# Kernel tuning notes

Measured on AMD Instinct MI355X. Metric: run time of the kernel, lower is better.

The kernel has to match this reference:

```python
import jax, jax.numpy as jnp
import numpy as np

B, R, NB, T = 32, 96, 5, 2048
FEAT_DIM = 64
SPARSITY = 0.2


def _per_band(X, community, W1, b1, W2, b2):
    # X: [R, T] wavelet coeffs for one (batch, band) slice
    n, t = X.shape
    f32 = X.dtype
    # --- functional connectivity (cosine of centered signals == Pearson corr) ---
    Xc = X - X.mean(axis=1, keepdims=True)
    norm = jnp.linalg.norm(Xc, axis=1, keepdims=True)
    norm = jnp.where(norm == 0, 1.0, norm)
    C = (Xc @ Xc.T) / (norm * norm.T)
    C = jnp.nan_to_num(C, nan=0.0)
    C = C * (1.0 - jnp.eye(n, dtype=f32))  # zero diagonal
    # --- quantile sparsification over strict lower triangle ---
    ti, tj = np.tril_indices(n, -1)
    thr = jnp.quantile(jnp.abs(C[ti, tj]), 1.0 - SPARSITY)
    A = C * (jnp.abs(C) >= thr).astype(f32)  # graph_type == 'weighted'
    # --- node features (5-dim, averaged over regions) ---
    mean_f = X.mean(axis=1)
    std_f = jnp.std(X, axis=1, ddof=1)  # torch.std is unbiased
    energy_f = (X ** 2).sum(axis=1)
    maxamp_f = jnp.abs(X).max(axis=1)
    ps = jnp.abs(jnp.fft.fft(X, axis=1)) ** 2
    ps = ps[:, : t // 2]
    s = ps.sum(axis=1, keepdims=True)
    s = jnp.where(s == 0, 1.0, s)
    p = ps / s
    ent_f = -(p * jnp.log(p + 1e-10)).sum(axis=1)
    node5 = jnp.stack([mean_f, std_f, energy_f, maxamp_f, ent_f], axis=1).mean(axis=0)
    # --- graph properties (6-dim) on binarized adjacency ---
    Bm = (A != 0).astype(f32)
    ne = Bm.sum() / 2.0
    density = ne / (n * (n - 1) / 2.0)
    deg = Bm.sum(axis=1)
    avg_deg = deg.mean()
    A2 = Bm @ Bm
    tri = (A2 * Bm).sum() / 6.0
    poss = (deg * (deg - 1.0)).sum() / 2.0
    clus = jnp.where(poss > 0, tri / jnp.where(poss > 0, poss, 1.0), 0.0)
    # global efficiency: safe reciprocal (zero where A+I == 0; original would emit inf)
    denom = Bm + jnp.eye(n, dtype=f32)
    eff = jnp.where(denom > 0, 1.0 / jnp.where(denom > 0, denom, 1.0), 0.0).sum() / (n * (n - 1))
    # approximate modularity with fixed 2-community assignment (deterministic)
    m2 = 2.0 * ne
    m2_safe = jnp.where(m2 > 0, m2, 1.0)
    same = (community[:, None] == community[None, :]) & (~jnp.eye(n, dtype=bool))
    expected = jnp.outer(deg, deg) / m2_safe
    mod = jnp.where(m2 > 0, (same * (Bm - expected)).sum() / m2_safe, 0.0)
    props = jnp.stack([ne, density, avg_deg, clus, eff, mod])
    feat11 = jnp.concatenate([node5, props])  # [11]
    # --- feature encoder MLP (dropout is identity at inference) ---
    h = jnp.maximum(feat11 @ W1.T + b1, 0.0)
    return A, h @ W2.T + b2


def _forward(wavelet_coeffs, frequency_bands, community, W1, b1, W2, b2):
    b, r, nb, t = wavelet_coeffs.shape
    Xs = wavelet_coeffs.transpose(0, 2, 1, 3).reshape(b * nb, r, t)  # [B*NB, R, T]
    A, F = jax.vmap(_per_band, in_axes=(0, None, None, None, None, None))(
        Xs, community, W1, b1, W2, b2)
    return A.reshape(b, nb, r, r), F.reshape(b, nb, -1)


def setup_inputs() -> dict:
    key = jax.random.key(0)
    k0, k1, k2, k3, k4 = jax.random.split(key, 5)
    wavelet_coeffs = jax.random.normal(k0, (B, R, NB, T), dtype=jnp.float32)
    frequency_bands = jax.random.uniform(k1, (NB, 2), dtype=jnp.float32)
    community = jax.random.randint(k2, (R,), 0, 2)
    W1 = jax.random.normal(k3, (32, 11), dtype=jnp.float32) * 0.3
    b1 = jnp.zeros((32,), jnp.float32)
    W2 = jax.random.normal(k4, (FEAT_DIM, 32), dtype=jnp.float32) * 0.18
    b2 = jnp.zeros((FEAT_DIM,), jnp.float32)
    return {"wavelet_coeffs": wavelet_coeffs, "frequency_bands": frequency_bands,
            "community": community, "W1": W1, "b1": b1, "W2": W2, "b2": b2}


def reference(wavelet_coeffs, frequency_bands, community, W1, b1, W2, b2):
    return _forward(wavelet_coeffs, frequency_bands, community, W1, b1, W2, b2)
```

## Files before the change

### kernel.cpp

```cpp
#include <hip/hip_runtime.h>
#include <hip/hip_bf16.h>
#include <math.h>
#include <float.h>

#ifndef M_PI
#define M_PI 3.14159265358979323846
#endif

#define NBANDS 160
#define RR 96
#define TT 2048
#define NTRIL 4560
#define A_ELEMS ((size_t)NBANDS * RR * RR)
#define NBIN 8192
#define MAXCAND 512
#define BKS 64
#define GPITCH 72
#define FBLK 384

#define PHI(L) ((L) ^ (((L) >> 5) & 31))

typedef float  f32x4  __attribute__((ext_vector_type(4)));
typedef __bf16 bf16x8 __attribute__((ext_vector_type(8)));
typedef __bf16 bf16x4 __attribute__((ext_vector_type(4)));

__device__ inline void blockReduceSum4(double v0, double v1, double v2, double v3,
                                       double* sred, double out[4]) {
    for (int off = 32; off > 0; off >>= 1) {
        v0 += __shfl_down(v0, off, 64);
        v1 += __shfl_down(v1, off, 64);
        v2 += __shfl_down(v2, off, 64);
        v3 += __shfl_down(v3, off, 64);
    }
    int lane = threadIdx.x & 63, wid = threadIdx.x >> 6;
    int nw = blockDim.x >> 6;
    if (lane == 0) {
        sred[wid * 4 + 0] = v0; sred[wid * 4 + 1] = v1;
        sred[wid * 4 + 2] = v2; sred[wid * 4 + 3] = v3;
    }
    __syncthreads();
    if (threadIdx.x < 4) {
        double r = sred[threadIdx.x];
        for (int w = 1; w < nw; w++) r += sred[w * 4 + threadIdx.x];
        sred[nw * 4 + threadIdx.x] = r;
    }
    __syncthreads();
    out[0] = sred[nw * 4 + 0]; out[1] = sred[nw * 4 + 1];
    out[2] = sred[nw * 4 + 2]; out[3] = sred[nw * 4 + 3];
    __syncthreads();
}

__device__ inline void blockReduceSum2(double v0, double v1,
                                       double* sred, double out[2]) {
    for (int off = 32; off > 0; off >>= 1) {
        v0 += __shfl_down(v0, off, 64);
        v1 += __shfl_down(v1, off, 64);
    }
    int lane = threadIdx.x & 63, wid = threadIdx.x >> 6;
    int nw = blockDim.x >> 6;
    if (lane == 0) { sred[wid * 2 + 0] = v0; sred[wid * 2 + 1] = v1; }
    __syncthreads();
    if (threadIdx.x < 2) {
        double r = sred[threadIdx.x];
        for (int w = 1; w < nw; w++) r += sred[w * 2 + threadIdx.x];
        sred[nw * 2 + threadIdx.x] = r;
    }
    __syncthreads();
    out[0] = sred[nw * 2 + 0]; out[1] = sred[nw * 2 + 1];
    __syncthreads();
}

__device__ inline void blockReduceMax2(double v0, double v1,
                                       double* sred, double out[2]) {
    for (int off = 32; off > 0; off >>= 1) {
        v0 = fmax(v0, __shfl_down(v0, off, 64));
        v1 = fmax(v1, __shfl_down(v1, off, 64));
    }
    int lane = threadIdx.x & 63, wid = threadIdx.x >> 6;
    int nw = blockDim.x >> 6;
    if (lane == 0) { sred[wid * 2 + 0] = v0; sred[wid * 2 + 1] = v1; }
    __syncthreads();
    if (threadIdx.x < 2) {
        double r = sred[threadIdx.x];
        for (int w = 1; w < nw; w++) r = fmax(r, sred[w * 2 + threadIdx.x]);
        sred[nw * 2 + threadIdx.x] = r;
    }
    __syncthreads();
    out[0] = sred[nw * 2 + 0]; out[1] = sred[nw * 2 + 1];
    __syncthreads();
}

__global__ void twiddle_kernel(float* tw) {
    int k = blockIdx.x * blockDim.x + threadIdx.x;
    if (k < 1024) {
        double ang = -2.0 * M_PI * (double)k / 2048.0;
        tw[2 * k]     = (float)cos(ang);
        tw[2 * k + 1] = (float)sin(ang);
    }
}

#define BFLY(r1, r2, WR, WI) do { \
    float _wr = (WR), _wi = (WI); \
    float _tr = _wr * yr[r2] - _wi * yi[r2]; \
    float _ti = _wr * yi[r2] + _wi * yr[r2]; \
    yr[r2] = yr[r1] - _tr; yi[r2] = yi[r1] - _ti; \
    yr[r1] += _tr; yi[r1] += _ti; } while (0)

__global__ __launch_bounds__(256) void rowstat_fft_kernel(
    const float* __restrict__ wc, const float* __restrict__ tw,
    double* __restrict__ rowstats)
{
    __shared__ float re[TT];
    __shared__ float im[TT];
    __shared__ double sred[32];
    __shared__ float bcast[4];

    int t = threadIdx.x;
    int g0 = blockIdx.x * 2;
    int g1 = g0 + 1;

    int band = g0 / RR, r0 = g0 % RR;
    int b = band / 5, nb = band % 5;
    size_t base0 = ((size_t)(b * RR + r0) * 5 + nb) * TT;
    size_t base1 = base0 + (size_t)5 * TT;
    const float2* twv = (const float2*)tw;

    float s0 = 0.f, s1 = 0.f, q0 = 0.f, q1 = 0.f, m0 = 0.f, m1 = 0.f;
#pragma unroll
    for (int c = 0; c < 8; c++) {
        int i = t + c * 256;
        float af = wc[base0 + i];
        float bf = wc[base1 + i];
        int P = PHI(i);
        re[P] = af; im[P] = bf;
        s0 += af; s1 += bf;
        q0 = fmaf(af, af, q0); q1 = fmaf(bf, bf, q1);
        m0 = fmaxf(m0, fabsf(af)); m1 = fmaxf(m1, fabsf(bf));
    }
    __syncthreads();

    double S4[4], M2[2];
    blockReduceSum4((double)s0, (double)s1, (double)q0, (double)q1, sred, S4);
    blockReduceMax2((double)m0, (double)m1, sred, M2);
    double SUM0 = S4[0], SUM1 = S4[1], SQ0 = S4[2], SQ1 = S4[3];
    double MX0 = M2[0], MX1 = M2[1];

    float yr[8], yi[8];

#pragma unroll
    for (int j = 0; j < 8; j++) {
        int p = 8 * t + j;
        int L = (int)(__brev((unsigned)p) >> 21);
        int P = PHI(L);
        yr[j] = re[P]; yi[j] = im[P];
    }

    const float RC = 0.70710678f;
    BFLY(0, 1, 1.0f, 0.0f); BFLY(2, 3, 1.0f, 0.0f);
    BFLY(4, 5, 1.0f, 0.0f); BFLY(6, 7, 1.0f, 0.0f);
    BFLY(0, 2, 1.0f, 0.0f); BFLY(1, 3, 0.0f, -1.0f);
    BFLY(4, 6, 1.0f, 0.0f); BFLY(5, 7, 0.0f, -1.0f);
    BFLY(0, 4, 1.0f, 0.0f); BFLY(1, 5, RC, -RC);
    BFLY(2, 6, 0.0f, -1.0f); BFLY(3, 7, -RC, -RC);

    __syncthreads();
#pragma unroll
    for (int j = 0; j < 8; j++) {
        int P = PHI(8 * t + j);
        re[P] = yr[j]; im[P] = yi[j];
    }
    __syncthreads();
    int oo = t & 7;
    int bb64 = 4 * ((t >> 3) & 7) + (t >> 6);
#pragma unroll
    for (int k = 0; k < 8; k++) {
        int P = PHI(64 * bb64 + 8 * k + oo);
        yr[k] = re[P]; yi[k] = im[P];
    }

    {
        float2 w0 = twv[oo << 7];
        BFLY(0, 1, w0.x, w0.y); BFLY(2, 3, w0.x, w0.y);
        BFLY(4, 5, w0.x, w0.y); BFLY(6, 7, w0.x, w0.y);
        float2 wa = twv[oo << 6];
        float2 wb = twv[(oo + 8) << 6];
        BFLY(0, 2, wa.x, wa.y); BFLY(1, 3, wb.x, wb.y);
        BFLY(4, 6, wa.x, wa.y); BFLY(5, 7, wb.x, wb.y);
        float2 wc0 = twv[oo << 5], wc1 = twv[(oo + 8) << 5];
        float2 wc2 = twv[(oo + 16) << 5], wc3 = twv[(oo + 24) << 5];
        BFLY(0, 4, wc0.x, wc0.y);
        BFLY(1, 5, wc1.x, wc1.y);
        BFLY(2, 6, wc2.x, wc2.y);
        BFLY(3, 7, wc3.x, wc3.y);
    }

    __syncthreads();
#pragma unroll
    for (int k = 0; k < 8; k++) {
        int P = PHI(64 * bb64 + 8 * k + oo);
        re[P] = yr[k]; im[P] = yi[k];
    }
    __syncthreads();
    int O3 = t & 63, Wq = t >> 6;
#pragma unroll
    for (int s = 0; s < 2; s++) {
        int B3 = Wq + 4 * s;
#pragma unroll
        for (int k = 0; k < 4; k++) {
            int P = PHI(256 * B3 + 64 * k + O3);
            yr[4 * s + k] = re[P]; yi[4 * s + k] = im[P];
        }
    }

    {
        float2 w0 = twv[O3 << 4];
        float2 wa = twv[O3 << 3];
        float2 wb = twv[(O3 + 64) << 3];
        BFLY(0, 1, w0.x, w0.y); BFLY(2, 3, w0.x, w0.y);
        BFLY(4, 5, w0.x, w0.y); BFLY(6, 7, w0.x, w0.y);
        BFLY(0, 2, wa.x, wa.y); BFLY(1, 3, wb.x, wb.y);
        BFLY(4, 6, wa.x, wa.y); BFLY(5, 7, wb.x, wb.y);
    }

    __syncthreads();
#pragma unroll
    for (int s = 0; s < 2; s++) {
        int B3 = Wq + 4 * s;
#pragma unroll
        for (int k = 0; k < 4; k++) {
            int P = PHI(256 * B3 + 64 * k + O3);
            re[P] = yr[4 * s + k]; im[P] = yi[4 * s + k];
        }
    }
    __syncthreads();
#pragma unroll
    for (int k = 0; k < 8; k++) {
        int P = PHI(256 * k + t);
        yr[k] = re[P]; yi[k] = im[P];
    }

    {
        float2 w0 = twv[t << 2];
        float2 wa = twv[t << 1];
        float2 wb = twv[(t + 256) << 1];
        BFLY(0, 1, w0.x, w0.y); BFLY(2, 3, w0.x, w0.y);
        BFLY(4, 5, w0.x, w0.y); BFLY(6, 7, w0.x, w0.y);
        BFLY(0, 2, wa.x, wa.y); BFLY(1, 3, wb.x, wb.y);
        BFLY(4, 6, wa.x, wa.y); BFLY(5, 7, wb.x, wb.y);
        float2 wf0 = twv[t], wf1 = twv[t + 256];
        float2 wf2 = twv[t + 512], wf3 = twv[t + 768];
        BFLY(0, 4, wf0.x, wf0.y);
        BFLY(1, 5, wf1.x, wf1.y);
        BFLY(2, 6, wf2.x, wf2.y);
        BFLY(3, 7, wf3.x, wf3.y);
    }

    __syncthreads();
#pragma unroll
    for (int k = 0; k < 8; k++) {
        int P = PHI(256 * k + t);
        re[P] = yr[k]; im[P] = yi[k];
    }
    __syncthreads();

    float psa[8], psb[8];
#pragma unroll
    for (int k = 0; k < 8; k++) {
        int q = (2048 - t - 256 * k) & 2047;
        int P = PHI(q);
        float prr = re[P], pii = im[P];
        float sr = yr[k] + prr, di = yi[k] - pii;
        float si = yi[k] + pii, dr = yr[k] - prr;
        psa[k] = 0.25f * (sr * sr + di * di);
        psb[k] = 0.25f * (si * si + dr * dr);
    }

    float la = 0.f, lb = 0.f;
#pragma unroll
    for (int k = 0; k < 8; k++) { la += psa[k]; lb += psb[k]; }
    double SS[2];
    blockReduceSum2((double)la, (double)lb, sred, SS);
    double SAall = SS[0], SBall = SS[1];
    if (t == 0) {
        bcast[0] = psa[0]; bcast[1] = psa[4];
        bcast[2] = psb[0]; bcast[3] = psb[4];
    }
    __syncthreads();
    double Sa = 0.5 * (SAall + (double)bcast[0] - (double)bcast[1]);
    double Sb = 0.5 * (SBall + (double)bcast[2] - (double)bcast[3]);
    if (Sa == 0.0) Sa = 1.0;
    if (Sb == 0.0) Sb = 1.0;
    float invSa = (float)(1.0 / Sa), invSb = (float)(1.0 / Sb);

    float ea = 0.f, eb = 0.f;
#pragma unroll
    for (int k = 0; k < 8; k++) {
        float pa = psa[k] * invSa;
        float pb = psb[k] * invSb;
        ea += pa * __logf(pa + 1e-10f);
        eb += pb * __logf(pb + 1e-10f);
    }
    double EE[2];
    blockReduceSum2((double)ea, (double)eb, sred, EE);
    double EAall = EE[0], EBall = EE[1];

    if (t == 0) {
        float pa0 = psa[0] * invSa, pa4 = psa[4] * invSa;
        float pb0 = psb[0] * invSb, pb4 = psb[4] * invSb;
        double TA = 0.5 * (EAall + (double)(pa0 * __logf(pa0 + 1e-10f))
                                 - (double)(pa4 * __logf(pa4 + 1e-10f)));
        double TB = 0.5 * (EBall + (double)(pb0 * __logf(pb0 + 1e-10f))
                                 - (double)(pb4 * __logf(pb4 + 1e-10f)));
        double mean0 = SUM0 / (double)TT;
        double mean1 = SUM1 / (double)TT;
        double nsq0 = SQ0 - (double)TT * mean0 * mean0; if (nsq0 < 0) nsq0 = 0;
        double nsq1 = SQ1 - (double)TT * mean1 * mean1; if (nsq1 < 0) nsq1 = 0;
        double* w0 = rowstats + (size_t)g0 * 6;
        double* w1 = rowstats + (size_t)g1 * 6;
        double n0 = sqrt(nsq0), n1 = sqrt(nsq1);
        w0[0] = mean0; w0[1] = (n0 == 0.0 ? 1.0 : n0); w0[2] = sqrt(nsq0 / 2047.0);
        w0[3] = SQ0;   w0[4] = MX0;                    w0[5] = -TA;
        w1[0] = mean1; w1[1] = (n1 == 0.0 ? 1.0 : n1); w1[2] = sqrt(nsq1 / 2047.0);
        w1[3] = SQ1;   w1[4] = MX1;                    w1[5] = -TB;
    }
}

#define CVW(v, row, c4) do { \
    __bf16 _h0 = (__bf16)v.x, _h1 = (__bf16)v.y, _h2 = (__bf16)v.z, _h3 = (__bf16)v.w; \
    __bf16 _l0 = (__bf16)(v.x - (float)_h0), _l1 = (__bf16)(v.y - (float)_h1); \
    __bf16 _l2 = (__bf16)(v.z - (float)_h2), _l3 = (__bf16)(v.w - (float)_h3); \
    *(bf16x4*)&sh_hi[row][(c4) * 4] = (bf16x4){_h0, _h1, _h2, _h3}; \
    *(bf16x4*)&sh_lo[row][(c4) * 4] = (bf16x4){_l0, _l1, _l2, _l3}; } while (0)

__global__ __launch_bounds__(FBLK) void fused_gram_finalize_kernel(
    const float* __restrict__ wc, const double* __restrict__ rowstats,
    const int* __restrict__ community,
    const float* __restrict__ W1, const float* __restrict__ b1,
    const float* __restrict__ W2, const float* __restrict__ b2,
    float* __restrict__ A_out, float* __restrict__ F_out)
{
    __shared__ __attribute__((aligned(16))) __bf16 sh_hi[RR][GPITCH];
    __shared__ __attribute__((aligned(16))) __bf16 sh_lo[RR][GPITCH];
    __shared__ float Cs[RR][RR];
    __shared__ int hist[NBIN];
    __shared__ int chunkv[256];
    __shared__ float cand[MAXCAND];
    __shared__ int ctrl[4];
    __shared__ double mean_s[RR], inv_s[RR];
    __shared__ int comm_s[RR];
    __shared__ unsigned long long msk[RR][2];
    __shared__ int deg[RR];
    __shared__ double sred[32];
    __shared__ double feat[11];
    __shared__ double hmlp[32];
    __shared__ double thr_s;

    int band = blockIdx.x, t = threadIdx.x;
    int b = band / 5, nb = band % 5;
    size_t bandbase = ((size_t)b * RR * 5 + nb) * TT;
    const double* rsb = rowstats + (size_t)band * RR * 6;

    if (t < RR) {
        mean_s[t] = rsb[t * 6 + 0];
        inv_s[t]  = 1.0 / rsb[t * 6 + 1];
        comm_s[t] = community[t];
    }
    for (int i = t; i < NBIN; i += FBLK) hist[i] = 0;
    if (t == 0) ctrl[3] = 0;

    int wave = t >> 6, lane = t & 63;
    int m16 = lane & 15, quad = lane >> 4;
    int arow = wave * 16 + m16;

    int gid0 = t, gid1 = t + 384, gid2 = t + 768, gid3 = t + 1152;
    int row0 = gid0 >> 4, c40 = gid0 & 15;
    int row1 = gid1 >> 4, c41 = gid1 & 15;
    int row2 = gid2 >> 4, c42 = gid2 & 15;
    int row3 = gid3 >> 4, c43 = gid3 & 15;
    const float* p0 = wc + bandbase + (size_t)row0 * (5 * TT) + c40 * 4;
    const float* p1 = wc + bandbase + (size_t)row1 * (5 * TT) + c41 * 4;
    const float* p2 = wc + bandbase + (size_t)row2 * (5 * TT) + c42 * 4;
    const float* p3 = wc + bandbase + (size_t)row3 * (5 * TT) + c43 * 4;

    f32x4 acc[6];
#pragma unroll
    for (int ct = 0; ct < 6; ct++) acc[ct] = (f32x4){0.f, 0.f, 0.f, 0.f};

    float4 pr0 = *(const float4*)(p0);
    float4 pr1 = *(const float4*)(p1);
    float4 pr2 = *(const float4*)(p2);
    float4 pr3 = *(const float4*)(p3);

    for (int st = 0; st < TT / BKS; st++) {
        CVW(pr0, row0, c40); CVW(pr1, row1, c41);
        CVW(pr2, row2, c42); CVW(pr3, row3, c43);
        __syncthreads();
        if (st + 1 < TT / BKS) {
            int k0 = (st + 1) * BKS;
            pr0 = *(const float4*)(p0 + k0);
            pr1 = *(const float4*)(p1 + k0);
            pr2 = *(const float4*)(p2 + k0);
            pr3 = *(const float4*)(p3 + k0);
        }
#pragma unroll
        for (int ks = 0; ks < BKS / 32; ks++) {
            int ko = ks * 32 + quad * 8;
            bf16x8 ah = *(const bf16x8*)&sh_hi[arow][ko];
            bf16x8 al = *(const bf16x8*)&sh_lo[arow][ko];
#pragma unroll
            for (int ct = 0; ct < 6; ct++) {
                int brow = ct * 16 + m16;
                bf16x8 bh = *(const bf16x8*)&sh_hi[brow][ko];
                bf16x8 bl = *(const bf16x8*)&sh_lo[brow][ko];
                acc[ct] = __builtin_amdgcn_mfma_f32_16x16x32_bf16(ah, bh, acc[ct], 0, 0, 0);
                acc[ct] = __builtin_amdgcn_mfma_f32_16x16x32_bf16(ah, bl, acc[ct], 0, 0, 0);
                acc[ct] = __builtin_amdgcn_mfma_f32_16x16x32_bf16(al, bh, acc[ct], 0, 0, 0);
            }
        }
        __syncthreads();
    }

#pragma unroll
    for (int ct = 0; ct < 6; ct++) {
#pragma unroll
        for (int r = 0; r < 4; r++) {
            int grow = wave * 16 + quad * 4 + r;
            int gcol = ct * 16 + m16;
            double cd = ((double)acc[ct][r]
                         - (double)TT * mean_s[grow] * mean_s[gcol])
                        * (inv_s[grow] * inv_s[gcol]);
            if (grow == gcol) cd = 0.0;
            float cf = (float)cd;
            Cs[grow][gcol] = cf;
            if (gcol < grow) {
                float val = fabsf(cf);
                int bin = (int)(val * (float)NBIN);
                bin = bin > (NBIN - 1) ? (NBIN - 1) : bin;
                atomicAdd(&hist[bin], 1);
            }
        }
    }
    __syncthreads();

    if (t < 256) {
        int cs = 0;
        for (int i = 0; i < NBIN / 256; i++) cs += hist[t * (NBIN / 256) + i];
        chunkv[t] = cs;
    }
    __syncthreads();

    if (t == 0) {
        int r0 = 3647, r1 = 3648;
        int cum = 0, c0 = 0;
        while (c0 < 256 && cum + chunkv[c0] <= r0) { cum += chunkv[c0]; c0++; }
        int bin = c0 * (NBIN / 256), cb = cum;
        while (cb + hist[bin] <= r0) { cb += hist[bin]; bin++; }
        int B0 = bin, cumB0 = cb;
        int bin1 = bin, cb1 = cb;
        while (cb1 + hist[bin1] <= r1) { cb1 += hist[bin1]; bin1++; }
        ctrl[0] = B0; ctrl[1] = bin1; ctrl[2] = cumB0;
    }
    __syncthreads();

    int B0 = ctrl[0], B1 = ctrl[1];
    for (int idx = t; idx < RR * RR; idx += FBLK) {
        int i = idx / RR, j = idx % RR;
        if (j < i) {
            float val = fabsf(Cs[i][j]);
            int bin = (int)(val * (float)NBIN);
            bin = bin > (NBIN - 1) ? (NBIN - 1) : bin;
            if (bin >= B0 && bin <= B1) {
                int k = atomicAdd(&ctrl[3], 1);
                if (k < MAXCAND) cand[k] = val;
            }
        }
    }
    __syncthreads();

    if (t == 0) {
        int n = ctrl[3]; if (n > MAXCAND) n = MAXCAND;
        for (int i = 1; i < n; i++) {
            float key = cand[i]; int j = i - 1;
            while (j >= 0 && cand[j] > key) { cand[j + 1] = cand[j]; j--; }
            cand[j + 1] = key;
        }
        int r0 = 3647 - ctrl[2];
        int r1 = 3648 - ctrl[2];
        double v0 = (double)cand[r0], v1 = (double)cand[r1];
        thr_s = v0 + 0.2 * (v1 - v0);
    }
    __syncthreads();
    double thr = thr_s;

    float* Ab = A_out + (size_t)band * (RR * RR);
    for (int idx = t; idx < RR * RR; idx += FBLK) {
        float cf = Cs[idx / RR][idx % RR];
        bool keep = ((double)fabsf(cf) >= thr);
        Ab[idx] = keep ? cf : 0.f;
    }

    for (int i = wave; i < RR; i += 6) {
        float vlo = Cs[i][lane];
        bool klo = ((double)fabsf(vlo) >= thr) && (vlo != 0.f);
        unsigned long long blo = __ballot(klo);
        float vhi = Cs[i][64 + (lane & 31)];
        bool khi = (lane < 32) && ((double)fabsf(vhi) >= thr) && (vhi != 0.f);
        unsigned long long bhi = __ballot(khi) & 0xffffffffull;
        if (lane == 0) {
            msk[i][0] = blo; msk[i][1] = bhi;
            deg[i] = __popcll(blo) + __popcll(bhi);
        }
    }
    __syncthreads();

    double triord = 0, ein = 0, expin = 0;
    for (int idx = t; idx < RR * RR; idx += FBLK) {
        int i = idx / RR, j = idx % RR;
        unsigned long long mi0 = msk[i][0], mi1 = msk[i][1];
        bool bij = (((j < 64) ? (mi0 >> j) : (mi1 >> (j - 64))) & 1ull) != 0;
        if (bij)
            triord += (double)(__popcll(mi0 & msk[j][0]) +
                               __popcll(mi1 & msk[j][1]));
        if (i != j && comm_s[i] == comm_s[j]) {
            ein += bij ? 1.0 : 0.0;
            expin += (double)deg[i] * (double)deg[j];
        }
    }
    double dv = (t < RR) ? (double)deg[t] : 0.0;
    double R1[4], R2[4], R3[2];
    blockReduceSum4(triord, ein, expin, dv, sred, R1);
    blockReduceSum4((t < RR) ? dv * (dv - 1.0) : 0.0,
                    (t < RR) ? rsb[t * 6 + 0] : 0.0,
                    (t < RR) ? rsb[t * 6 + 2] : 0.0,
                    (t < RR) ? rsb[t * 6 + 3] : 0.0, sred, R2);
    blockReduceSum2((t < RR) ? rsb[t * 6 + 4] : 0.0,
                    (t < RR) ? rsb[t * 6 + 5] : 0.0, sred, R3);
    double TRI = R1[0], EIN = R1[1], EXPIN = R1[2], DEGS = R1[3];
    double POSS2 = R2[0], N0 = R2[1], N1 = R2[2], N2 = R2[3];
    double N3 = R3[0], N4 = R3[1];

    if (t == 0) {
        double ne = 0.5 * DEGS;
        feat[0] = N0 / (double)RR;
        feat[1] = N1 / (double)RR;
        feat[2] = N2 / (double)RR;
        feat[3] = N3 / (double)RR;
        feat[4] = N4 / (double)RR;
        feat[5] = ne;
        feat[6] = ne / (double)NTRIL;
        feat[7] = DEGS / (double)RR;
        double tri = TRI / 6.0, poss = POSS2 * 0.5;
        feat[8] = (poss > 0.0) ? tri / poss : 0.0;
        feat[9] = ((double)RR + DEGS) / ((double)RR * (double)(RR - 1));
        double m2 = DEGS;
        feat[10] = (m2 > 0.0) ? (EIN - EXPIN / m2) / m2 : 0.0;
    }
    __syncthreads();

    if (t < 32) {
        double a = (double)b1[t];
        for (int k = 0; k < 11; k++) a += (double)W1[t * 11 + k] * feat[k];
        hmlp[t] = (a > 0.0) ? a : 0.0;
    }
    __syncthreads();
    if (t < 64) {
        double a = (double)b2[t];
        for (int j = 0; j < 32; j++) a += (double)W2[t * 32 + j] * hmlp[j];
        F_out[(size_t)band * 64 + t] = (float)a;
    }
}

extern "C" void kernel_launch(void* const* d_in, const int* in_sizes, int n_in,
                              void* d_out, int out_size, void* d_ws, size_t ws_size,
                              hipStream_t stream) {
    const float* wc        = (const float*)d_in[0];
    const int*   community = (const int*)d_in[2];
    const float* W1        = (const float*)d_in[3];
    const float* b1        = (const float*)d_in[4];
    const float* W2        = (const float*)d_in[5];
    const float* b2        = (const float*)d_in[6];

    float* A_out = (float*)d_out;
    float* F_out = A_out + A_ELEMS;

    char* ws = (char*)d_ws;
    float*  tw       = (float*)ws;
    double* rowstats = (double*)(ws + 8192);

    hipLaunchKernelGGL(twiddle_kernel, dim3(4), dim3(256), 0, stream, tw);
    hipLaunchKernelGGL(rowstat_fft_kernel, dim3(NBANDS * RR / 2), dim3(256), 0, stream,
                       wc, tw, rowstats);
    hipLaunchKernelGGL(fused_gram_finalize_kernel, dim3(NBANDS), dim3(FBLK), 0, stream,
                       wc, rowstats, community, W1, b1, W2, b2, A_out, F_out);
}
```

Measured before the change: 304.2 us.

## Double-buffer gram LDS tiles, parallelize quantile bin search and candidate selection

The gram loop now keeps two LDS buffers, so the next k-slice is converted and stored while MFMAs run on the current one, removing one barrier per stage. The serial single-thread histogram prefix walk becomes a wave-level scan plus parallel bin lookup. The insertion sort of quantile candidates is replaced by a parallel rank count. The FFT row-stat kernel is also split into two half-grid launches, which adds launch overhead and does not obviously help. These changes add shared memory per block, and the rank count is quadratic in the candidate count.

```diff
diff --git a/kernel.cpp b/kernel.cpp
--- a/kernel.cpp
+++ b/kernel.cpp
@@ -15,6 +15,7 @@
 #define NBIN 8192
 #define MAXCAND 512
 #define BKS 64
+#define NST (TT / BKS)
 #define GPITCH 72
 #define FBLK 384
 
@@ -108,7 +109,7 @@
 
 __global__ __launch_bounds__(256) void rowstat_fft_kernel(
     const float* __restrict__ wc, const float* __restrict__ tw,
-    double* __restrict__ rowstats)
+    double* __restrict__ rowstats, int goff)
 {
     __shared__ float re[TT];
     __shared__ float im[TT];
@@ -116,7 +117,7 @@
     __shared__ float bcast[4];
 
     int t = threadIdx.x;
-    int g0 = blockIdx.x * 2;
+    int g0 = (blockIdx.x + goff) * 2;
     int g1 = g0 + 1;
 
     int band = g0 / RR, r0 = g0 % RR;
@@ -325,12 +326,12 @@
     }
 }
 
-#define CVW(v, row, c4) do { \
+#define CVW(BUF, v, row, c4) do { \
     __bf16 _h0 = (__bf16)v.x, _h1 = (__bf16)v.y, _h2 = (__bf16)v.z, _h3 = (__bf16)v.w; \
     __bf16 _l0 = (__bf16)(v.x - (float)_h0), _l1 = (__bf16)(v.y - (float)_h1); \
     __bf16 _l2 = (__bf16)(v.z - (float)_h2), _l3 = (__bf16)(v.w - (float)_h3); \
-    *(bf16x4*)&sh_hi[row][(c4) * 4] = (bf16x4){_h0, _h1, _h2, _h3}; \
-    *(bf16x4*)&sh_lo[row][(c4) * 4] = (bf16x4){_l0, _l1, _l2, _l3}; } while (0)
+    *(bf16x4*)&sh_hi[BUF][row][(c4) * 4] = (bf16x4){_h0, _h1, _h2, _h3}; \
+    *(bf16x4*)&sh_lo[BUF][row][(c4) * 4] = (bf16x4){_l0, _l1, _l2, _l3}; } while (0)
 
 __global__ __launch_bounds__(FBLK) void fused_gram_finalize_kernel(
     const float* __restrict__ wc, const double* __restrict__ rowstats,
@@ -339,13 +340,16 @@
     const float* __restrict__ W2, const float* __restrict__ b2,
     float* __restrict__ A_out, float* __restrict__ F_out)
 {
-    __shared__ __attribute__((aligned(16))) __bf16 sh_hi[RR][GPITCH];
-    __shared__ __attribute__((aligned(16))) __bf16 sh_lo[RR][GPITCH];
+    __shared__ __attribute__((aligned(16))) __bf16 sh_hi[2][RR][GPITCH];
+    __shared__ __attribute__((aligned(16))) __bf16 sh_lo[2][RR][GPITCH];
     __shared__ float Cs[RR][RR];
     __shared__ int hist[NBIN];
     __shared__ int chunkv[256];
+    __shared__ int pchunk[256];
+    __shared__ int gpre_s[64];
     __shared__ float cand[MAXCAND];
-    __shared__ int ctrl[4];
+    __shared__ int ctrl[8];
+    __shared__ float selv[2];
     __shared__ double mean_s[RR], inv_s[RR];
     __shared__ int comm_s[RR];
     __shared__ unsigned long long msk[RR][2];
@@ -372,11 +376,10 @@
     int m16 = lane & 15, quad = lane >> 4;
     int arow = wave * 16 + m16;
 
-    int gid0 = t, gid1 = t + 384, gid2 = t + 768, gid3 = t + 1152;
-    int row0 = gid0 >> 4, c40 = gid0 & 15;
-    int row1 = gid1 >> 4, c41 = gid1 & 15;
-    int row2 = gid2 >> 4, c42 = gid2 & 15;
-    int row3 = gid3 >> 4, c43 = gid3 & 15;
+    int row0 = t >> 4,           c40 = t & 15;
+    int row1 = (t + 384) >> 4,   c41 = (t + 384) & 15;
+    int row2 = (t + 768) >> 4,   c42 = (t + 768) & 15;
+    int row3 = (t + 1152) >> 4,  c43 = (t + 1152) & 15;
     const float* p0 = wc + bandbase + (size_t)row0 * (5 * TT) + c40 * 4;
     const float* p1 = wc + bandbase + (size_t)row1 * (5 * TT) + c41 * 4;
     const float* p2 = wc + bandbase + (size_t)row2 * (5 * TT) + c42 * 4;
@@ -386,36 +389,46 @@
 #pragma unroll
     for (int ct = 0; ct < 6; ct++) acc[ct] = (f32x4){0.f, 0.f, 0.f, 0.f};
 
-    float4 pr0 = *(const float4*)(p0);
-    float4 pr1 = *(const float4*)(p1);
-    float4 pr2 = *(const float4*)(p2);
-    float4 pr3 = *(const float4*)(p3);
-
-    for (int st = 0; st < TT / BKS; st++) {
-        CVW(pr0, row0, c40); CVW(pr1, row1, c41);
-        CVW(pr2, row2, c42); CVW(pr3, row3, c43);
-        __syncthreads();
-        if (st + 1 < TT / BKS) {
+    {
+        float4 v0 = *(const float4*)(p0);
+        float4 v1 = *(const float4*)(p1);
+        float4 v2 = *(const float4*)(p2);
+        float4 v3 = *(const float4*)(p3);
+        CVW(0, v0, row0, c40); CVW(0, v1, row1, c41);
+        CVW(0, v2, row2, c42); CVW(0, v3, row3, c43);
+    }
+    __syncthreads();
+
+    for (int st = 0; st < NST; st++) {
+        int cur = st & 1;
+        float4 q0, q1, q2, q3;
+        bool more = (st + 1 < NST);
+        if (more) {
             int k0 = (st + 1) * BKS;
-            pr0 = *(const float4*)(p0 + k0);
-            pr1 = *(const float4*)(p1 + k0);
-            pr2 = *(const float4*)(p2 + k0);
-            pr3 = *(const float4*)(p3 + k0);
+            q0 = *(const float4*)(p0 + k0);
+            q1 = *(const float4*)(p1 + k0);
+            q2 = *(const float4*)(p2 + k0);
+            q3 = *(const float4*)(p3 + k0);
         }
 #pragma unroll
         for (int ks = 0; ks < BKS / 32; ks++) {
             int ko = ks * 32 + quad * 8;
-            bf16x8 ah = *(const bf16x8*)&sh_hi[arow][ko];
-            bf16x8 al = *(const bf16x8*)&sh_lo[arow][ko];
+            bf16x8 ah = *(const bf16x8*)&sh_hi[cur][arow][ko];
+            bf16x8 al = *(const bf16x8*)&sh_lo[cur][arow][ko];
 #pragma unroll
             for (int ct = 0; ct < 6; ct++) {
                 int brow = ct * 16 + m16;
-                bf16x8 bh = *(const bf16x8*)&sh_hi[brow][ko];
-                bf16x8 bl = *(const bf16x8*)&sh_lo[brow][ko];
+                bf16x8 bh = *(const bf16x8*)&sh_hi[cur][brow][ko];
+                bf16x8 bl = *(const bf16x8*)&sh_lo[cur][brow][ko];
                 acc[ct] = __builtin_amdgcn_mfma_f32_16x16x32_bf16(ah, bh, acc[ct], 0, 0, 0);
                 acc[ct] = __builtin_amdgcn_mfma_f32_16x16x32_bf16(ah, bl, acc[ct], 0, 0, 0);
                 acc[ct] = __builtin_amdgcn_mfma_f32_16x16x32_bf16(al, bh, acc[ct], 0, 0, 0);
             }
+        }
+        if (more) {
+            int nxt = cur ^ 1;
+            CVW(nxt, q0, row0, c40); CVW(nxt, q1, row1, c41);
+            CVW(nxt, q2, row2, c42); CVW(nxt, q3, row3, c43);
         }
         __syncthreads();
     }
@@ -444,21 +457,49 @@
 
     if (t < 256) {
         int cs = 0;
+#pragma unroll
         for (int i = 0; i < NBIN / 256; i++) cs += hist[t * (NBIN / 256) + i];
         chunkv[t] = cs;
     }
     __syncthreads();
-
-    if (t == 0) {
-        int r0 = 3647, r1 = 3648;
-        int cum = 0, c0 = 0;
-        while (c0 < 256 && cum + chunkv[c0] <= r0) { cum += chunkv[c0]; c0++; }
-        int bin = c0 * (NBIN / 256), cb = cum;
-        while (cb + hist[bin] <= r0) { cb += hist[bin]; bin++; }
-        int B0 = bin, cumB0 = cb;
-        int bin1 = bin, cb1 = cb;
-        while (cb1 + hist[bin1] <= r1) { cb1 += hist[bin1]; bin1++; }
-        ctrl[0] = B0; ctrl[1] = bin1; ctrl[2] = cumB0;
+    if (t < 64) {
+        int s4 = chunkv[4 * t] + chunkv[4 * t + 1] + chunkv[4 * t + 2] + chunkv[4 * t + 3];
+        int inc = s4;
+        for (int d = 1; d < 64; d <<= 1) {
+            int u = __shfl_up(inc, d, 64);
+            if (t >= d) inc += u;
+        }
+        gpre_s[t] = inc - s4;
+    }
+    __syncthreads();
+    if (t < 256) {
+        int base = gpre_s[t >> 2];
+        for (int j = (t & ~3); j < t; j++) base += chunkv[j];
+        pchunk[t] = base;
+    }
+    __syncthreads();
+    if (t < 256) {
+        int lo = pchunk[t], hi2 = lo + chunkv[t];
+        if (lo <= 3647 && 3647 < hi2) ctrl[4] = t;
+        if (lo <= 3648 && 3648 < hi2) ctrl[5] = t;
+    }
+    __syncthreads();
+    {
+        int c0 = ctrl[4], c1 = ctrl[5];
+        if (t < 32) {
+            int binb = c0 * 32;
+            int pre = pchunk[c0];
+            for (int j = 0; j < t; j++) pre += hist[binb + j];
+            int cnt = hist[binb + t];
+            if (pre <= 3647 && 3647 < pre + cnt) { ctrl[0] = binb + t; ctrl[2] = pre; }
+        } else if (t < 64) {
+            int tt2 = t - 32;
+            int binb = c1 * 32;
+            int pre = pchunk[c1];
+            for (int j = 0; j < tt2; j++) pre += hist[binb + j];
+            int cnt = hist[binb + tt2];
+            if (pre <= 3648 && 3648 < pre + cnt) ctrl[1] = binb + tt2;
+        }
     }
     __syncthreads();
 
@@ -477,16 +518,24 @@
     }
     __syncthreads();
 
+    {
+        int n = ctrl[3]; if (n > MAXCAND) n = MAXCAND;
+        int r0l = 3647 - ctrl[2];
+        int r1l = 3648 - ctrl[2];
+        for (int i = t; i < n; i += FBLK) {
+            float v = cand[i];
+            int rank = 0;
+            for (int j = 0; j < n; j++) {
+                float u = cand[j];
+                rank += (u < v || (u == v && j < i)) ? 1 : 0;
+            }
+            if (rank == r0l) selv[0] = v;
+            if (rank == r1l) selv[1] = v;
+        }
+    }
+    __syncthreads();
     if (t == 0) {
-        int n = ctrl[3]; if (n > MAXCAND) n = MAXCAND;
-        for (int i = 1; i < n; i++) {
-            float key = cand[i]; int j = i - 1;
-            while (j >= 0 && cand[j] > key) { cand[j + 1] = cand[j]; j--; }
-            cand[j + 1] = key;
-        }
-        int r0 = 3647 - ctrl[2];
-        int r1 = 3648 - ctrl[2];
-        double v0 = (double)cand[r0], v1 = (double)cand[r1];
+        double v0 = (double)selv[0], v1 = (double)selv[1];
         thr_s = v0 + 0.2 * (v1 - v0);
     }
     __syncthreads();
@@ -527,17 +576,17 @@
         }
     }
     double dv = (t < RR) ? (double)deg[t] : 0.0;
-    double R1[4], R2[4], R3[2];
-    blockReduceSum4(triord, ein, expin, dv, sred, R1);
+    double R1v[4], R2v[4], R3v[2];
+    blockReduceSum4(triord, ein, expin, dv, sred, R1v);
     blockReduceSum4((t < RR) ? dv * (dv - 1.0) : 0.0,
                     (t < RR) ? rsb[t * 6 + 0] : 0.0,
                     (t < RR) ? rsb[t * 6 + 2] : 0.0,
-                    (t < RR) ? rsb[t * 6 + 3] : 0.0, sred, R2);
+                    (t < RR) ? rsb[t * 6 + 3] : 0.0, sred, R2v);
     blockReduceSum2((t < RR) ? rsb[t * 6 + 4] : 0.0,
-                    (t < RR) ? rsb[t * 6 + 5] : 0.0, sred, R3);
-    double TRI = R1[0], EIN = R1[1], EXPIN = R1[2], DEGS = R1[3];
-    double POSS2 = R2[0], N0 = R2[1], N1 = R2[2], N2 = R2[3];
-    double N3 = R3[0], N4 = R3[1];
+                    (t < RR) ? rsb[t * 6 + 5] : 0.0, sred, R3v);
+    double TRI = R1v[0], EIN = R1v[1], EXPIN = R1v[2], DEGS = R1v[3];
+    double POSS2 = R2v[0], N0 = R2v[1], N1 = R2v[2], N2 = R2v[3];
+    double N3 = R3v[0], N4 = R3v[1];
 
     if (t == 0) {
         double ne = 0.5 * DEGS;
@@ -587,9 +636,12 @@
     float*  tw       = (float*)ws;
     double* rowstats = (double*)(ws + 8192);
 
+    const int HGRID = NBANDS * RR / 4;
     hipLaunchKernelGGL(twiddle_kernel, dim3(4), dim3(256), 0, stream, tw);
-    hipLaunchKernelGGL(rowstat_fft_kernel, dim3(NBANDS * RR / 2), dim3(256), 0, stream,
-                       wc, tw, rowstats);
+    hipLaunchKernelGGL(rowstat_fft_kernel, dim3(HGRID), dim3(256), 0, stream,
+                       wc, tw, rowstats, 0);
+    hipLaunchKernelGGL(rowstat_fft_kernel, dim3(HGRID), dim3(256), 0, stream,
+                       wc, tw, rowstats, HGRID);
     hipLaunchKernelGGL(fused_gram_finalize_kernel, dim3(NBANDS), dim3(FBLK), 0, stream,
                        wc, rowstats, community, W1, b1, W2, b2, A_out, F_out);
 }
```

New measurement: 316.0 us. 3.9% more time.
